# Kernel optimization log

Measured on AMD Instinct MI355X. Metric: run time of the kernel, lower is better.

## Reference

```python
import jax, jax.numpy as jnp
import numpy as np

D_MODEL, D_STATE, D_CONV, EXPAND = 1024, 16, 4, 2
D_INNER = EXPAND * D_MODEL
BATCH, SEQ = 2, 2048


def setup_inputs() -> dict:
    key = jax.random.key(0)
    ks = jax.random.split(key, 10)
    inv = lambda n: 1.0 / np.sqrt(n)
    return {
        "x": jax.random.normal(ks[0], (BATCH, SEQ, D_MODEL), jnp.float32),
        "in_proj_w": jax.random.uniform(ks[1], (2 * D_INNER, D_MODEL), jnp.float32, -inv(D_MODEL), inv(D_MODEL)),
        "conv_w": jax.random.uniform(ks[2], (D_INNER, D_INNER, D_CONV), jnp.float32, -inv(D_INNER * D_CONV), inv(D_INNER * D_CONV)),
        "conv_b": jax.random.uniform(ks[3], (D_INNER,), jnp.float32, -inv(D_INNER * D_CONV), inv(D_INNER * D_CONV)),
        "dt_w": jax.random.uniform(ks[4], (D_INNER, D_INNER), jnp.float32, -inv(D_INNER), inv(D_INNER)),
        "dt_b": jax.random.uniform(ks[5], (D_INNER,), jnp.float32, -inv(D_INNER), inv(D_INNER)),
        "A_log": jax.random.normal(ks[6], (D_INNER, D_STATE), jnp.float32) * 0.01,
        "D": jnp.ones((D_INNER,), jnp.float32),
        "B_w": jax.random.uniform(ks[7], (D_STATE, D_INNER), jnp.float32, -inv(D_INNER), inv(D_INNER)),
        "C_w": jax.random.uniform(ks[8], (D_STATE, D_INNER), jnp.float32, -inv(D_INNER), inv(D_INNER)),
        "out_w": jax.random.uniform(ks[9], (D_MODEL, D_INNER), jnp.float32, -inv(D_INNER), inv(D_INNER)),
    }


def _forward(x, in_proj_w, conv_w, conv_b, dt_w, dt_b, A_log, D, B_w, C_w, out_w):
    xz = x @ in_proj_w.T                      # [b, l, 2*d_inner]
    xc, z = jnp.split(xz, 2, axis=-1)
    # causal depthful conv1d (full channel mixing, left-padded)
    h = jnp.transpose(xc, (0, 2, 1))          # [b, d, l]
    h = jnp.pad(h, ((0, 0), (0, 0), (D_CONV - 1, 0)))
    h = jax.lax.conv_general_dilated(h, conv_w, (1,), 'VALID',
                                     dimension_numbers=('NCH', 'OIH', 'NCH'))
    h = h + conv_b[None, :, None]
    u = jnp.transpose(h, (0, 2, 1))           # [b, l, d_inner]

    dt = jnp.clip(jax.nn.sigmoid(u @ dt_w.T + dt_b), 1e-4, 1.0)  # [b, l, d]
    A = -jnp.exp(A_log)                       # [d, n]
    Bm = u @ B_w.T                            # [b, l, n]
    Cm = u @ C_w.T                            # [b, l, n]

    # time-major scan over the recurrence
    u_t = jnp.transpose(u, (1, 0, 2))
    dt_t = jnp.transpose(dt, (1, 0, 2))
    B_t = jnp.transpose(Bm, (1, 0, 2))
    C_t = jnp.transpose(Cm, (1, 0, 2))

    def step(state, inp):
        ut, dtt, bt, ct = inp                 # [b,d], [b,d], [b,n], [b,n]
        dA = jnp.exp(jnp.clip(dtt[:, :, None] * A, -5.0, 5.0))   # [b,d,n]
        dB = dtt[:, :, None] * bt[:, None, :] * ut[:, :, None]   # [b,d,n]
        state = dA * state + dB + 1e-6
        y = jnp.sum(state * ct[:, None, :], axis=-1) + D * ut    # [b,d]
        return state, y

    state0 = jnp.zeros((x.shape[0], D_INNER, D_STATE), x.dtype)
    _, ys = jax.lax.scan(step, state0, (u_t, dt_t, B_t, C_t))
    y = jnp.transpose(ys, (1, 0, 2))          # [b, l, d_inner]
    y = y * jax.nn.silu(z)
    return y @ out_w.T                        # [b, l, d_model]


def reference(x, in_proj_w, conv_w, conv_b, dt_w, dt_b, A_log, D, B_w, C_w, out_w):
    return _forward(x, in_proj_w, conv_w, conv_b, dt_w, dt_b, A_log, D, B_w, C_w, out_w)
```

## Files before the change

kernel.cpp:

```cpp
#include <hip/hip_runtime.h>

#define BATCHN 2
#define SEQL   2048
#define DM     1024
#define DI     2048
#define DSN    16
#define MTOT   (BATCHN * SEQL)
#define PADL   (SEQL + 3)
#define NC     64
#define CL     (SEQL / NC)

typedef __attribute__((ext_vector_type(8))) __bf16 bf16x8;
typedef __attribute__((ext_vector_type(4))) float f32x4;

__device__ __forceinline__ unsigned short f2b(float f) {
    union { float f; unsigned u; } v; v.f = f;
    unsigned r = v.u + 0x7FFF + ((v.u >> 16) & 1);
    return (unsigned short)(r >> 16);
}
__device__ __forceinline__ float b2f(unsigned short b) {
    union { float f; unsigned u; } v; v.u = ((unsigned)b) << 16;
    return v.f;
}

__device__ __forceinline__ void gl_lds16(const void* g, void* l) {
    __builtin_amdgcn_global_load_lds(
        (const __attribute__((address_space(1))) unsigned int*)g,
        (__attribute__((address_space(3))) unsigned int*)l, 16, 0, 0);
}

__device__ __forceinline__ void swz(int& bx, int& by) {
    int gx = gridDim.x, gy = gridDim.y;
    int lin = blockIdx.y * gx + blockIdx.x;
    int xcd = lin & 7, k = lin >> 3;
    int rw = gx >> 1, rh = gy >> 2;
    by = (xcd >> 1) * rh + k / rw;
    bx = (xcd & 1) * rw + k % rw;
}

__global__ void cvt_f32_bf16(const float* __restrict__ src, unsigned short* __restrict__ dst, int n4) {
    int i = blockIdx.x * blockDim.x + threadIdx.x;
    if (i < n4) {
        float4 v = ((const float4*)src)[i];
        ushort4 o;
        o.x = f2b(v.x); o.y = f2b(v.y); o.z = f2b(v.z); o.w = f2b(v.w);
        ((ushort4*)dst)[i] = o;
    }
}

__global__ void cvt_x_pad(const float* __restrict__ src, unsigned short* __restrict__ dst) {
    int i = blockIdx.x * blockDim.x + threadIdx.x;
    if (i < MTOT * DM / 4) {
        int b = i >> 19;
        float4 v = ((const float4*)src)[i];
        ushort4 o;
        o.x = f2b(v.x); o.y = f2b(v.y); o.z = f2b(v.z); o.w = f2b(v.w);
        ((ushort4*)dst)[i + (b + 1) * (3 * DM / 4)] = o;
    }
}

__global__ void cvt_convw(const float* __restrict__ cw, unsigned short* __restrict__ wk) {
    int i = blockIdx.x * blockDim.x + threadIdx.x;
    if (i < DI * DI) {
        float4 v = ((const float4*)cw)[i];
        wk[0 * (size_t)DI * DI + i] = f2b(v.x);
        wk[1 * (size_t)DI * DI + i] = f2b(v.y);
        wk[2 * (size_t)DI * DI + i] = f2b(v.z);
        wk[3 * (size_t)DI * DI + i] = f2b(v.w);
    }
}

__global__ void __launch_bounds__(256)
tp_cvt(const float* __restrict__ src, unsigned short* __restrict__ dst) {
    __shared__ float tile[32][33];
    int ct = blockIdx.x * 32, it = blockIdx.y * 32;
    int tx = threadIdx.x & 31, ty = threadIdx.x >> 5;
#pragma unroll
    for (int r = 0; r < 4; ++r)
        tile[ty + r * 8][tx] = src[(size_t)(it + ty + r * 8) * DM + ct + tx];
    __syncthreads();
#pragma unroll
    for (int r = 0; r < 4; ++r)
        dst[(size_t)(ct + ty + r * 8) * DI + it + tx] = f2b(tile[tx][ty + r * 8]);
}

__global__ void zero_pad(unsigned short* __restrict__ xpad) {
    int i = blockIdx.x * blockDim.x + threadIdx.x;
    if (i < BATCHN * 3 * DM) {
        int b = i / (3 * DM);
        int r = i % (3 * DM);
        xpad[(size_t)b * PADL * DM + r] = 0;
    }
}

template<int MODE>
__global__ void __launch_bounds__(256)
gemm_bt(const unsigned short* __restrict__ Abase,
        const unsigned short* __restrict__ Bbase,
        const float* __restrict__ bias,
        unsigned short* __restrict__ out_bf,
        float* __restrict__ out_f,
        int K)
{
    __shared__ __align__(16) unsigned short As[128 * 64];
    __shared__ __align__(16) unsigned short Bs[128 * 64];

    const int t = threadIdx.x;
    const int lane = t & 63;
    const int wave = t >> 6;
    const int wm = wave & 1, wn = wave >> 1;
    int bx, by;
    swz(bx, by);
    const int m0 = by * 128, n0 = bx * 128;
    const int srow = t >> 3;
    const int scol = (t & 7) * 8;
    const int gcol = (((t & 7) ^ (srow & 7))) * 8;

    f32x4 acc[4][4];
#pragma unroll
    for (int i = 0; i < 4; ++i)
#pragma unroll
        for (int j = 0; j < 4; ++j)
            acc[i][j] = f32x4{0.f, 0.f, 0.f, 0.f};

    const int nseg = (MODE == 1) ? 4 : 1;
    for (int seg = 0; seg < nseg; ++seg) {
        const unsigned short* arow[4];
        const unsigned short* brow[4];
#pragma unroll
        for (int i = 0; i < 4; ++i) {
            int rg = m0 + srow + i * 32;
            if (MODE == 0) {
                arow[i] = Abase + ((size_t)(rg >> 11) * PADL + 3 + (rg & 2047)) * DM;
            } else if (MODE == 1) {
                arow[i] = Abase + ((size_t)(rg >> 11) * PADL + (rg & 2047) + seg) * DM;
            } else if (MODE == 4) {
                arow[i] = Abase + (size_t)blockIdx.z * DI * DI + (size_t)rg * K;
            } else {
                arow[i] = Abase + (size_t)rg * K;
            }
            int ng = n0 + srow + i * 32;
            if (MODE == 1)
                brow[i] = Bbase + (size_t)seg * DI * DM + (size_t)ng * DM;
            else
                brow[i] = Bbase + (size_t)ng * K;
        }
        const int Kseg = (MODE == 1) ? DM : K;
        for (int k0 = 0; k0 < Kseg; k0 += 64) {
#pragma unroll
            for (int i = 0; i < 4; ++i)
                gl_lds16(arow[i] + k0 + gcol, &As[(size_t)(srow + i * 32) * 64 + scol]);
#pragma unroll
            for (int i = 0; i < 4; ++i)
                gl_lds16(brow[i] + k0 + gcol, &Bs[(size_t)(srow + i * 32) * 64 + scol]);
            __syncthreads();
            const int qa = (lane >> 4) * 8;
            const int am = lane & 15;
            const int sw = (am & 7) << 3;
#pragma unroll
            for (int kk = 0; kk < 64; kk += 32) {
                bf16x8 af[4], bfv[4];
#pragma unroll
                for (int i = 0; i < 4; ++i)
                    af[i] = *(const bf16x8*)&As[(wm * 64 + i * 16 + am) * 64 + ((kk + qa) ^ sw)];
#pragma unroll
                for (int j = 0; j < 4; ++j)
                    bfv[j] = *(const bf16x8*)&Bs[(wn * 64 + j * 16 + am) * 64 + ((kk + qa) ^ sw)];
#pragma unroll
                for (int i = 0; i < 4; ++i)
#pragma unroll
                    for (int j = 0; j < 4; ++j)
                        acc[i][j] = __builtin_amdgcn_mfma_f32_16x16x32_bf16(
                            af[i], bfv[j], acc[i][j], 0, 0, 0);
            }
            __syncthreads();
        }
    }

    const int erow0 = m0 + wm * 64;
    const int ecol0 = n0 + wn * 64 + (lane & 15);
    const int rq = (lane >> 4) * 4;
#pragma unroll
    for (int i = 0; i < 4; ++i) {
#pragma unroll
        for (int j = 0; j < 4; ++j) {
            int col = ecol0 + j * 16;
#pragma unroll
            for (int r = 0; r < 4; ++r) {
                int row = erow0 + i * 16 + rq + r;
                float v = acc[i][j][r];
                if (MODE == 0) {
                    out_bf[(size_t)row * DI + col] = f2b(v);
                } else if (MODE == 1) {
                    v += bias[col];
                    out_bf[(size_t)row * DI + col] = f2b(v);
                } else if (MODE == 2) {
                    v += bias[col];
                    float s = 1.f / (1.f + __expf(-v));
                    s = fminf(fmaxf(s, 1e-4f), 1.f);
                    out_f[(size_t)row * DI + col] = s;
                } else if (MODE == 3) {
                    out_f[(size_t)row * DM + col] = v;
                } else {
                    out_bf[(size_t)blockIdx.z * DI * DM + (size_t)row * DM + col] = f2b(v);
                }
            }
        }
    }
}

__global__ void __launch_bounds__(256)
bc_gemm(const unsigned short* __restrict__ u,
        const unsigned short* __restrict__ w,
        float* __restrict__ outf)
{
    int t = threadIdx.x;
    int n = t & 31;
    int r = blockIdx.x * 8 + (t >> 5);
    const unsigned short* up = u + (size_t)r * DI;
    const unsigned short* wp = w + (size_t)n * DI;
    float acc = 0.f;
    for (int k0 = 0; k0 < DI; k0 += 8) {
        bf16x8 uv = *(const bf16x8*)(up + k0);
        bf16x8 wv = *(const bf16x8*)(wp + k0);
#pragma unroll
        for (int j = 0; j < 8; ++j)
            acc += (float)uv[j] * (float)wv[j];
    }
    outf[(size_t)r * 32 + n] = acc;
}

__global__ void __launch_bounds__(256)
scan_p1(const float* __restrict__ dtf,
        const unsigned short* __restrict__ u_bf,
        const float* __restrict__ bcf,
        const float* __restrict__ A_log,
        float* __restrict__ Pbuf,
        float* __restrict__ Sbuf)
{
    const int t = threadIdx.x;
    const int blk = blockIdx.x;
    const int c  = blk & (NC - 1);
    const int dh = (blk >> 6) & 7;
    const int b  = blk >> 9;
    const int d  = dh * 256 + t;

    float Adn[16];
    {
        const float4* ar = (const float4*)(A_log + (size_t)d * DSN);
#pragma unroll
        for (int q = 0; q < 4; ++q) {
            float4 v = ar[q];
            Adn[q * 4 + 0] = -__expf(v.x);
            Adn[q * 4 + 1] = -__expf(v.y);
            Adn[q * 4 + 2] = -__expf(v.z);
            Adn[q * 4 + 3] = -__expf(v.w);
        }
    }
    float s[16], P[16];
#pragma unroll
    for (int n = 0; n < 16; ++n) { s[n] = 0.f; P[n] = 1.f; }

    const size_t rowbase = (size_t)b * SEQL + (size_t)c * CL;
    for (int l0 = 0; l0 < CL; l0 += 4) {
        float dt4[4], u4[4];
#pragma unroll
        for (int j = 0; j < 4; ++j) {
            size_t rb = rowbase + l0 + j;
            dt4[j] = dtf[rb * DI + d];
            u4[j] = b2f(u_bf[rb * DI + d]);
        }
#pragma unroll
        for (int j = 0; j < 4; ++j) {
            size_t rb = rowbase + l0 + j;
            const float4* Br = (const float4*)(bcf + rb * 32);
            float Bn[16];
#pragma unroll
            for (int q = 0; q < 4; ++q) {
                float4 v = Br[q];
                Bn[q * 4 + 0] = v.x; Bn[q * 4 + 1] = v.y;
                Bn[q * 4 + 2] = v.z; Bn[q * 4 + 3] = v.w;
            }
            float dt = dt4[j];
            float dBu = dt * u4[j];
#pragma unroll
            for (int n = 0; n < 16; ++n) {
                float x = dt * Adn[n];
                x = fminf(fmaxf(x, -5.f), 5.f);
                float dA = __expf(x);
                P[n] *= dA;
                s[n] = dA * s[n] + (dBu * Bn[n] + 1e-6f);
            }
        }
    }
    size_t ob = (((size_t)c * BATCHN + b) * DI + d) * DSN;
#pragma unroll
    for (int q = 0; q < 4; ++q) {
        ((float4*)(Pbuf + ob))[q] = make_float4(P[q*4], P[q*4+1], P[q*4+2], P[q*4+3]);
        ((float4*)(Sbuf + ob))[q] = make_float4(s[q*4], s[q*4+1], s[q*4+2], s[q*4+3]);
    }
}

__global__ void __launch_bounds__(256)
scan_p2(const float* __restrict__ Pbuf,
        const float* __restrict__ Sbuf,
        float* __restrict__ Ibuf)
{
    const int i = blockIdx.x * 256 + threadIdx.x;
    const int stride = BATCHN * DI * DSN;
    float s = 0.f;
    for (int c0 = 0; c0 < NC; c0 += 8) {
        float Pv[8], Sv[8];
#pragma unroll
        for (int j = 0; j < 8; ++j) {
            size_t idx = (size_t)(c0 + j) * stride + i;
            Pv[j] = Pbuf[idx];
            Sv[j] = Sbuf[idx];
        }
#pragma unroll
        for (int j = 0; j < 8; ++j) {
            size_t idx = (size_t)(c0 + j) * stride + i;
            Ibuf[idx] = s;
            s = Pv[j] * s + Sv[j];
        }
    }
}

__global__ void __launch_bounds__(256)
scan_p3(const float* __restrict__ dtf,
        const unsigned short* __restrict__ u_bf,
        const float* __restrict__ bcf,
        const unsigned short* __restrict__ z_bf,
        const float* __restrict__ A_log,
        const float* __restrict__ Dvec,
        const float* __restrict__ Ibuf,
        unsigned short* __restrict__ y_bf)
{
    const int t = threadIdx.x;
    const int blk = blockIdx.x;
    const int c  = blk & (NC - 1);
    const int dh = (blk >> 6) & 7;
    const int b  = blk >> 9;
    const int d  = dh * 256 + t;

    float Adn[16];
    {
        const float4* ar = (const float4*)(A_log + (size_t)d * DSN);
#pragma unroll
        for (int q = 0; q < 4; ++q) {
            float4 v = ar[q];
            Adn[q * 4 + 0] = -__expf(v.x);
            Adn[q * 4 + 1] = -__expf(v.y);
            Adn[q * 4 + 2] = -__expf(v.z);
            Adn[q * 4 + 3] = -__expf(v.w);
        }
    }
    const float Dd = Dvec[d];
    float s[16];
    {
        size_t ib = (((size_t)c * BATCHN + b) * DI + d) * DSN;
#pragma unroll
        for (int q = 0; q < 4; ++q) {
            float4 v = ((const float4*)(Ibuf + ib))[q];
            s[q * 4 + 0] = v.x; s[q * 4 + 1] = v.y;
            s[q * 4 + 2] = v.z; s[q * 4 + 3] = v.w;
        }
    }

    const size_t rowbase = (size_t)b * SEQL + (size_t)c * CL;
    for (int l0 = 0; l0 < CL; l0 += 4) {
        float dt4[4], u4[4], z4[4];
#pragma unroll
        for (int j = 0; j < 4; ++j) {
            size_t rb = rowbase + l0 + j;
            dt4[j] = dtf[rb * DI + d];
            u4[j] = b2f(u_bf[rb * DI + d]);
            z4[j] = b2f(z_bf[rb * DI + d]);
        }
#pragma unroll
        for (int j = 0; j < 4; ++j) {
            size_t rb = rowbase + l0 + j;
            const float4* Br = (const float4*)(bcf + rb * 32);
            float Bn[16], Cn[16];
#pragma unroll
            for (int q = 0; q < 4; ++q) {
                float4 v = Br[q];
                Bn[q * 4 + 0] = v.x; Bn[q * 4 + 1] = v.y;
                Bn[q * 4 + 2] = v.z; Bn[q * 4 + 3] = v.w;
                float4 w = Br[q + 4];
                Cn[q * 4 + 0] = w.x; Cn[q * 4 + 1] = w.y;
                Cn[q * 4 + 2] = w.z; Cn[q * 4 + 3] = w.w;
            }
            float dt = dt4[j];
            float dBu = dt * u4[j];
            float y = 0.f;
#pragma unroll
            for (int n = 0; n < 16; ++n) {
                float x = dt * Adn[n];
                x = fminf(fmaxf(x, -5.f), 5.f);
                float dA = __expf(x);
                s[n] = dA * s[n] + (dBu * Bn[n] + 1e-6f);
                y += s[n] * Cn[n];
            }
            y += Dd * u4[j];
            float zz = z4[j];
            y *= zz / (1.f + __expf(-zz));
            y_bf[rb * DI + d] = f2b(y);
        }
    }
}

extern "C" void kernel_launch(void* const* d_in, const int* in_sizes, int n_in,
                              void* d_out, int out_size, void* d_ws, size_t ws_size,
                              hipStream_t stream) {
    const float* x     = (const float*)d_in[0];
    const float* ipw   = (const float*)d_in[1];
    const float* convw = (const float*)d_in[2];
    const float* convb = (const float*)d_in[3];
    const float* dtw   = (const float*)d_in[4];
    const float* dtb   = (const float*)d_in[5];
    const float* alog  = (const float*)d_in[6];
    const float* dvec  = (const float*)d_in[7];
    const float* bw    = (const float*)d_in[8];
    const float* cwm   = (const float*)d_in[9];
    const float* ow    = (const float*)d_in[10];
    float* out = (float*)d_out;

    char* ws = (char*)d_ws;
    size_t off = 0;
    auto carve = [&](size_t bytes) {
        char* p = ws + off;
        off += (bytes + 255) & ~(size_t)255;
        return p;
    };
    unsigned short* xpad   = (unsigned short*)carve((size_t)BATCHN * PADL * DM * 2);
    unsigned short* ipz_bf = (unsigned short*)carve((size_t)DI * DM * 2);
    unsigned short* Pt_bf  = (unsigned short*)carve((size_t)DM * DI * 2);
    unsigned short* wk_bf  = (unsigned short*)carve((size_t)4 * DI * DI * 2);
    unsigned short* mk_bf  = (unsigned short*)carve((size_t)4 * DI * DM * 2);
    unsigned short* dtw_bf = (unsigned short*)carve((size_t)DI * DI * 2);
    unsigned short* ow_bf  = (unsigned short*)carve((size_t)DM * DI * 2);
    unsigned short* bc_bf  = (unsigned short*)carve((size_t)2 * DSN * DI * 2);
    unsigned short* z_bf   = (unsigned short*)carve((size_t)MTOT * DI * 2);
    unsigned short* u_bf   = (unsigned short*)carve((size_t)MTOT * DI * 2);
    float*          dt_f   = (float*)carve((size_t)MTOT * DI * 4);
    float*          bc_f   = (float*)carve((size_t)MTOT * 2 * DSN * 4);
    unsigned short* y_bf   = (unsigned short*)carve((size_t)MTOT * DI * 2);
    float*          Pbuf   = (float*)carve((size_t)NC * BATCHN * DI * DSN * 4);
    float*          Sbuf   = (float*)carve((size_t)NC * BATCHN * DI * DSN * 4);
    float*          Ibuf   = (float*)carve((size_t)NC * BATCHN * DI * DSN * 4);

    cvt_x_pad<<<MTOT * DM / 4 / 256, 256, 0, stream>>>(x, xpad);
    zero_pad<<<(BATCHN * 3 * DM + 255) / 256, 256, 0, stream>>>(xpad);
    cvt_convw<<<DI * DI / 256, 256, 0, stream>>>(convw, wk_bf);
    tp_cvt<<<dim3(DM / 32, DI / 32), 256, 0, stream>>>(ipw, Pt_bf);
    cvt_f32_bf16<<<DI * DM / 4 / 256, 256, 0, stream>>>(ipw + (size_t)DI * DM, ipz_bf, DI * DM / 4);
    cvt_f32_bf16<<<DI * DI / 4 / 256, 256, 0, stream>>>(dtw, dtw_bf, DI * DI / 4);
    cvt_f32_bf16<<<DM * DI / 4 / 256, 256, 0, stream>>>(ow, ow_bf, DM * DI / 4);
    cvt_f32_bf16<<<(DSN * DI / 4 + 255) / 256, 256, 0, stream>>>(bw, bc_bf, DSN * DI / 4);
    cvt_f32_bf16<<<(DSN * DI / 4 + 255) / 256, 256, 0, stream>>>(cwm, bc_bf + (size_t)DSN * DI, DSN * DI / 4);

    gemm_bt<4><<<dim3(8, 16, 4), 256, 0, stream>>>(wk_bf, Pt_bf, nullptr, mk_bf, nullptr, DI);
    gemm_bt<0><<<dim3(16, 32), 256, 0, stream>>>(xpad, ipz_bf, nullptr, z_bf, nullptr, DM);
    gemm_bt<1><<<dim3(16, 32), 256, 0, stream>>>(xpad, mk_bf, convb, u_bf, nullptr, DM);
    bc_gemm<<<MTOT / 8, 256, 0, stream>>>(u_bf, bc_bf, bc_f);
    gemm_bt<2><<<dim3(16, 32), 256, 0, stream>>>(u_bf, dtw_bf, dtb, nullptr, dt_f, DI);
    scan_p1<<<BATCHN * 8 * NC, 256, 0, stream>>>(dt_f, u_bf, bc_f, alog, Pbuf, Sbuf);
    scan_p2<<<BATCHN * DI * DSN / 256, 256, 0, stream>>>(Pbuf, Sbuf, Ibuf);
    scan_p3<<<BATCHN * 8 * NC, 256, 0, stream>>>(dt_f, u_bf, bc_f, z_bf, alog, dvec, Ibuf, y_bf);
    gemm_bt<3><<<dim3(8, 32), 256, 0, stream>>>(y_bf, ow_bf, nullptr, nullptr, out, DI);
}
```

Before: 548.0 us.

## Replace scalar B/C projection GEMM with split-K MFMA kernel plus reduction

The small u@[B_w;C_w]^T projection (N=32, K=2048) was computed with a scalar dot-product kernel, one thread per output. It now uses bf16 MFMA 16x16x32 instructions, with K split into 8 chunks across the grid so there are enough blocks. Partial sums go to a new scratch buffer and a second kernel reduces them. This trades scalar FMA throughput for matrix cores, at the cost of one extra launch and extra global traffic for the partials.

```diff
diff --git a/kernel.cpp b/kernel.cpp
--- a/kernel.cpp
+++ b/kernel.cpp
@@ -9,6 +9,7 @@
 #define PADL   (SEQL + 3)
 #define NC     64
 #define CL     (SEQL / NC)
+#define BCKS   8
 
 typedef __attribute__((ext_vector_type(8))) __bf16 bf16x8;
 typedef __attribute__((ext_vector_type(4))) float f32x4;
@@ -210,24 +211,66 @@
 }
 
 __global__ void __launch_bounds__(256)
-bc_gemm(const unsigned short* __restrict__ u,
+bc_mfma(const unsigned short* __restrict__ u,
         const unsigned short* __restrict__ w,
-        float* __restrict__ outf)
+        float* __restrict__ pc)
 {
-    int t = threadIdx.x;
-    int n = t & 31;
-    int r = blockIdx.x * 8 + (t >> 5);
-    const unsigned short* up = u + (size_t)r * DI;
-    const unsigned short* wp = w + (size_t)n * DI;
-    float acc = 0.f;
-    for (int k0 = 0; k0 < DI; k0 += 8) {
-        bf16x8 uv = *(const bf16x8*)(up + k0);
-        bf16x8 wv = *(const bf16x8*)(wp + k0);
-#pragma unroll
-        for (int j = 0; j < 8; ++j)
-            acc += (float)uv[j] * (float)wv[j];
-    }
-    outf[(size_t)r * 32 + n] = acc;
+    const int t = threadIdx.x;
+    const int lane = t & 63;
+    const int wave = t >> 6;
+    const int ks = blockIdx.x;
+    const int m0 = blockIdx.y * 128 + wave * 32;
+    const int am = lane & 15, quad = lane >> 4;
+
+    f32x4 acc[2][2];
+#pragma unroll
+    for (int i = 0; i < 2; ++i)
+#pragma unroll
+        for (int j = 0; j < 2; ++j)
+            acc[i][j] = f32x4{0.f, 0.f, 0.f, 0.f};
+
+    const int kbase = ks * (DI / BCKS);
+    const unsigned short* ur0 = u + (size_t)(m0 + am) * DI;
+    const unsigned short* ur1 = u + (size_t)(m0 + 16 + am) * DI;
+    const unsigned short* wr0 = w + (size_t)am * DI;
+    const unsigned short* wr1 = w + (size_t)(16 + am) * DI;
+#pragma unroll 2
+    for (int kk = 0; kk < DI / BCKS; kk += 32) {
+        int k = kbase + kk + quad * 8;
+        bf16x8 a0 = *(const bf16x8*)(ur0 + k);
+        bf16x8 a1 = *(const bf16x8*)(ur1 + k);
+        bf16x8 b0 = *(const bf16x8*)(wr0 + k);
+        bf16x8 b1 = *(const bf16x8*)(wr1 + k);
+        acc[0][0] = __builtin_amdgcn_mfma_f32_16x16x32_bf16(a0, b0, acc[0][0], 0, 0, 0);
+        acc[0][1] = __builtin_amdgcn_mfma_f32_16x16x32_bf16(a0, b1, acc[0][1], 0, 0, 0);
+        acc[1][0] = __builtin_amdgcn_mfma_f32_16x16x32_bf16(a1, b0, acc[1][0], 0, 0, 0);
+        acc[1][1] = __builtin_amdgcn_mfma_f32_16x16x32_bf16(a1, b1, acc[1][1], 0, 0, 0);
+    }
+    float* base = pc + (size_t)ks * MTOT * 32;
+#pragma unroll
+    for (int i = 0; i < 2; ++i)
+#pragma unroll
+        for (int j = 0; j < 2; ++j)
+#pragma unroll
+            for (int r = 0; r < 4; ++r) {
+                int row = m0 + i * 16 + quad * 4 + r;
+                int col = j * 16 + am;
+                base[(size_t)row * 32 + col] = acc[i][j][r];
+            }
+}
+
+__global__ void __launch_bounds__(256)
+bc_reduce(const float* __restrict__ pc, float* __restrict__ outf)
+{
+    int i = blockIdx.x * 256 + threadIdx.x;
+    const float4* p4 = (const float4*)pc;
+    float4 s = p4[i];
+#pragma unroll
+    for (int ks = 1; ks < BCKS; ++ks) {
+        float4 v = p4[(size_t)ks * (MTOT * 8) + i];
+        s.x += v.x; s.y += v.y; s.z += v.z; s.w += v.w;
+    }
+    ((float4*)outf)[i] = s;
 }
 
 __global__ void __launch_bounds__(256)
@@ -449,6 +492,7 @@
     float*          Pbuf   = (float*)carve((size_t)NC * BATCHN * DI * DSN * 4);
     float*          Sbuf   = (float*)carve((size_t)NC * BATCHN * DI * DSN * 4);
     float*          Ibuf   = (float*)carve((size_t)NC * BATCHN * DI * DSN * 4);
+    float*          pc_f   = (float*)carve((size_t)BCKS * MTOT * 32 * 4);
 
     cvt_x_pad<<<MTOT * DM / 4 / 256, 256, 0, stream>>>(x, xpad);
     zero_pad<<<(BATCHN * 3 * DM + 255) / 256, 256, 0, stream>>>(xpad);
@@ -463,7 +507,8 @@
     gemm_bt<4><<<dim3(8, 16, 4), 256, 0, stream>>>(wk_bf, Pt_bf, nullptr, mk_bf, nullptr, DI);
     gemm_bt<0><<<dim3(16, 32), 256, 0, stream>>>(xpad, ipz_bf, nullptr, z_bf, nullptr, DM);
     gemm_bt<1><<<dim3(16, 32), 256, 0, stream>>>(xpad, mk_bf, convb, u_bf, nullptr, DM);
-    bc_gemm<<<MTOT / 8, 256, 0, stream>>>(u_bf, bc_bf, bc_f);
+    bc_mfma<<<dim3(BCKS, MTOT / 128), 256, 0, stream>>>(u_bf, bc_bf, pc_f);
+    bc_reduce<<<MTOT * 32 / 4 / 256, 256, 0, stream>>>(pc_f, bc_f);
     gemm_bt<2><<<dim3(16, 32), 256, 0, stream>>>(u_bf, dtw_bf, dtb, nullptr, dt_f, DI);
     scan_p1<<<BATCHN * 8 * NC, 256, 0, stream>>>(dt_f, u_bf, bc_f, alog, Pbuf, Sbuf);
     scan_p2<<<BATCHN * DI * DSN / 256, 256, 0, stream>>>(Pbuf, Sbuf, Ibuf);
```

After: 487.1 us. -11.1%, faster.
